# Performance work log

Measured on AMD Instinct MI355X. Metric: run time of the kernel, lower is better.

The kernel has to match this reference:

```python
import jax, jax.numpy as jnp
import numpy as np

N_TOKEN = 267735
D_EMBED = 1024
D_PROJ = 1024
CUTOFF_ENDS = [0, 20000, 40000, 200000, N_TOKEN]
DIV_VAL = 4
INIT_STD = 0.02


def setup_inputs() -> dict:
    key = jax.random.key(0)
    ks = jax.random.split(key, 9)
    inp = jax.random.randint(ks[0], (8, 4096), 0, N_TOKEN, dtype=jnp.int64)
    out = {"inp": inp}
    for i in range(4):
        l, r = CUTOFF_ENDS[i], CUTOFF_ENDS[i + 1]
        d_emb_i = D_EMBED // (DIV_VAL ** i)
        out[f"emb{i}"] = jax.random.normal(ks[1 + i], (r - l, d_emb_i), dtype=jnp.float32) * INIT_STD
        out[f"proj{i}"] = jax.random.normal(ks[5 + i], (d_emb_i, D_PROJ), dtype=jnp.float32) * INIT_STD
    return out


def reference(inp, emb0, emb1, emb2, emb3, proj0, proj1, proj2, proj3):
    embs = [emb0, emb1, emb2, emb3]
    projs = [proj0, proj1, proj2, proj3]
    flat = inp.reshape(-1)  # [N]
    out = jnp.zeros((flat.shape[0], D_PROJ), dtype=jnp.float32)
    for i in range(4):
        l, r = CUTOFF_ENDS[i], CUTOFF_ENDS[i + 1]
        mask = (flat >= l) & (flat < r)  # [N]
        idx = jnp.clip(flat - l, 0, r - l - 1)  # in-range even for out-of-bucket tokens
        e = embs[i][idx]                         # [N, d_emb_i] gather
        p = jnp.einsum('id,de->ie', e, projs[i])  # [N, D_PROJ]
        out = out + jnp.where(mask[:, None], p, 0.0)
    emb_scale = D_PROJ ** 0.5
    return (out * emb_scale).reshape(inp.shape + (D_PROJ,))
```

## Files before the change

kernel.cpp:

```cpp
#include <hip/hip_runtime.h>
#include <hip/hip_bf16.h>

#define N_TOK   32768
#define DPROJ   1024
#define SCALE   32.0f

typedef short bf16x8 __attribute__((ext_vector_type(8)));
typedef float f32x4  __attribute__((ext_vector_type(4)));

__device__ __forceinline__ short f2bf(float f) {
    unsigned u = __builtin_bit_cast(unsigned, f);
    unsigned r = (u + 0x7FFFu + ((u >> 16) & 1u)) >> 16;
    return (short)r;
}

__global__ void k_prep(const int* __restrict__ inp, int* __restrict__ cnt,
                       int* __restrict__ perm, int* __restrict__ rowidx,
                       const float* __restrict__ p0, const float* __restrict__ p1,
                       const float* __restrict__ p2, const float* __restrict__ p3,
                       short* __restrict__ t0, short* __restrict__ t1,
                       short* __restrict__ t2, short* __restrict__ t3)
{
    __shared__ float tile[128][17];

    if (blockIdx.x < 128) {
        int i = blockIdx.x * 256 + threadIdx.x;
        int t = inp[i];
        int b, l;
        if (t < 20000)       { b = 0; l = 0; }
        else if (t < 40000)  { b = 1; l = 20000; }
        else if (t < 200000) { b = 2; l = 40000; }
        else                 { b = 3; l = 200000; }

        unsigned long long m0 = __ballot(b == 0);
        unsigned long long m1 = __ballot(b == 1);
        unsigned long long m2 = __ballot(b == 2);
        unsigned long long m3 = __ballot(b == 3);

        int lane = threadIdx.x & 63;
        int mybase = 0;
        if (lane < 4) {
            unsigned long long mm = (lane == 0) ? m0 : (lane == 1) ? m1 : (lane == 2) ? m2 : m3;
            mybase = atomicAdd(&cnt[lane], __popcll(mm));
        }
        int base = __shfl(mybase, b);
        unsigned long long mine = (b == 0) ? m0 : (b == 1) ? m1 : (b == 2) ? m2 : m3;
        unsigned long long lt = (lane == 0) ? 0ull : (~0ull >> (64 - lane));
        int pos = base + __popcll(mine & lt);
        perm[b * N_TOK + pos]   = i;
        rowidx[b * N_TOK + pos] = t - l;
        return;
    }

    int bid = blockIdx.x - 128;
    const float* src; short* dst; int K; int rel;
    if (bid < 512)      { src = p0; dst = t0; K = 1024; rel = bid; }
    else if (bid < 640) { src = p1; dst = t1; K = 256;  rel = bid - 512; }
    else if (bid < 704) { src = p2; dst = t2; K = 64;   rel = bid - 640; }
    else                { src = p3; dst = t3; K = 16;   rel = bid - 704; }
    int ktiles = (K + 127) >> 7;
    int k0 = (rel % ktiles) * 128;
    int n0 = (rel / ktiles) * 16;
    int t = threadIdx.x;

    #pragma unroll
    for (int i = 0; i < 2; ++i) {
        int idx = t + i * 256;
        int k = idx >> 2;
        int nc = (idx & 3) * 4;
        if (k0 + k < K) {
            float4 v = *reinterpret_cast<const float4*>(src + (size_t)(k0 + k) * DPROJ + n0 + nc);
            tile[k][nc + 0] = v.x; tile[k][nc + 1] = v.y;
            tile[k][nc + 2] = v.z; tile[k][nc + 3] = v.w;
        }
    }
    __syncthreads();
    int n  = t >> 4;
    int kc = (t & 15) * 8;
    if (k0 + kc < K) {
        short s[8];
        #pragma unroll
        for (int j = 0; j < 8; ++j) s[j] = f2bf(tile[kc + j][n]);
        *reinterpret_cast<int4*>(dst + (size_t)(n0 + n) * K + k0 + kc) =
            *reinterpret_cast<const int4*>(s);
    }
}

__global__ __launch_bounds__(256, 2) void k_gemm(
    const float* __restrict__ e0, const float* __restrict__ e1,
    const float* __restrict__ e2, const float* __restrict__ e3,
    const short* __restrict__ t0, const short* __restrict__ t1,
    const short* __restrict__ t2, const short* __restrict__ t3,
    const int* __restrict__ cnt, const int* __restrict__ perm,
    const int* __restrict__ rowidx, float* __restrict__ out)
{
    __shared__ short As[64][40];
    __shared__ short Bs[256][40];

    const int hw     = blockIdx.y * 4 + blockIdx.x;
    const int ytile  = (hw >> 5) * 8 + (hw & 7);
    const int panel  = (hw >> 3) & 3;

    const int c0 = cnt[0], c1 = cnt[1], c2 = cnt[2], c3 = cnt[3];
    const int q0 = (c0 + 63) & ~63;
    const int q1 = q0 + ((c1 + 63) & ~63);
    const int q2 = q1 + ((c2 + 63) & ~63);
    const int q3 = q2 + ((c3 + 63) & ~63);
    const int p0 = ytile * 64;
    if (p0 >= q3) return;
    int b, M, m0, K; const float* emb; const short* bt;
    if (p0 < q0)      { b = 0; M = c0; m0 = p0;      K = 1024; emb = e0; bt = t0; }
    else if (p0 < q1) { b = 1; M = c1; m0 = p0 - q0; K = 256;  emb = e1; bt = t1; }
    else if (p0 < q2) { b = 2; M = c2; m0 = p0 - q1; K = 64;   emb = e2; bt = t2; }
    else              { b = 3; M = c3; m0 = p0 - q2; K = 16;   emb = e3; bt = t3; }
    if (m0 >= M) return;
    const int* pperm = perm   + b * N_TOK;
    const int* prow  = rowidx + b * N_TOK;

    const int tid  = threadIdx.x;
    const int lane = tid & 63;
    const int w    = tid >> 6;
    const int n0   = panel * 256;

    const int sr = tid >> 2;
    const int sc = (tid & 3) * 8;
    const bool avalid = (m0 + sr) < M;
    const int  arow   = avalid ? prow[m0 + sr] : 0;
    const float* aptr = emb + (size_t)arow * K;

    f32x4 acc[4][4];
    #pragma unroll
    for (int mi = 0; mi < 4; ++mi)
        #pragma unroll
        for (int ni = 0; ni < 4; ++ni) acc[mi][ni] = (f32x4)0.0f;

    const int koff = (lane >> 4) * 8;
    const int fr   = lane & 15;

    float av[8];
    int4  bv[4];
#define ISSUE_LOADS(K0)                                                        \
    {                                                                          \
        _Pragma("unroll")                                                      \
        for (int j = 0; j < 8; ++j) av[j] = 0.0f;                              \
        if (avalid && ((K0) + sc) < K) {                                       \
            float4 x = *reinterpret_cast<const float4*>(aptr + (K0) + sc);     \
            float4 y = *reinterpret_cast<const float4*>(aptr + (K0) + sc + 4); \
            av[0] = x.x; av[1] = x.y; av[2] = x.z; av[3] = x.w;                \
            av[4] = y.x; av[5] = y.y; av[6] = y.z; av[7] = y.w;                \
        }                                                                      \
        _Pragma("unroll")                                                      \
        for (int g = 0; g < 4; ++g) {                                          \
            if (((K0) + sc) < K)                                               \
                bv[g] = *reinterpret_cast<const int4*>(                        \
                    bt + (size_t)(n0 + g * 64 + sr) * K + (K0) + sc);          \
            else bv[g] = make_int4(0, 0, 0, 0);                                \
        }                                                                      \
    }

    ISSUE_LOADS(0);
    for (int k0 = 0; k0 < K; k0 += 32) {
        __syncthreads();
        {
            short asv[8];
            #pragma unroll
            for (int j = 0; j < 8; ++j) asv[j] = f2bf(av[j]);
            *reinterpret_cast<int4*>(&As[sr][sc]) = *reinterpret_cast<const int4*>(asv);
            #pragma unroll
            for (int g = 0; g < 4; ++g)
                *reinterpret_cast<int4*>(&Bs[g * 64 + sr][sc]) = bv[g];
        }
        if (k0 + 32 < K) ISSUE_LOADS(k0 + 32);
        __syncthreads();

        bf16x8 afr[4], bfr[4];
        #pragma unroll
        for (int mi = 0; mi < 4; ++mi)
            afr[mi] = *reinterpret_cast<const bf16x8*>(&As[mi * 16 + fr][koff]);
        #pragma unroll
        for (int ni = 0; ni < 4; ++ni)
            bfr[ni] = *reinterpret_cast<const bf16x8*>(&Bs[w * 64 + ni * 16 + fr][koff]);
        #pragma unroll
        for (int mi = 0; mi < 4; ++mi)
            #pragma unroll
            for (int ni = 0; ni < 4; ++ni)
                acc[mi][ni] = __builtin_amdgcn_mfma_f32_16x16x32_bf16(
                    afr[mi], bfr[ni], acc[mi][ni], 0, 0, 0);
    }
#undef ISSUE_LOADS

    const int colb = n0 + w * 64 + fr;
    const int rowg = (lane >> 4) * 4;
    #pragma unroll
    for (int mi = 0; mi < 4; ++mi) {
        #pragma unroll
        for (int j = 0; j < 4; ++j) {
            int m = m0 + mi * 16 + rowg + j;
            if (m < M) {
                size_t r = (size_t)pperm[m] * DPROJ + colb;
                out[r]      = acc[mi][0][j] * SCALE;
                out[r + 16] = acc[mi][1][j] * SCALE;
                out[r + 32] = acc[mi][2][j] * SCALE;
                out[r + 48] = acc[mi][3][j] * SCALE;
            }
        }
    }
}

__global__ void k_naive(const int* __restrict__ inp,
                        const float* __restrict__ emb0, const float* __restrict__ emb1,
                        const float* __restrict__ emb2, const float* __restrict__ emb3,
                        const float* __restrict__ proj0, const float* __restrict__ proj1,
                        const float* __restrict__ proj2, const float* __restrict__ proj3,
                        float* __restrict__ out)
{
    __shared__ float e[1024];
    int t = inp[blockIdx.x];
    const float* emb; const float* proj; int K, l;
    if (t < 20000)       { emb = emb0; proj = proj0; K = 1024; l = 0; }
    else if (t < 40000)  { emb = emb1; proj = proj1; K = 256;  l = 20000; }
    else if (t < 200000) { emb = emb2; proj = proj2; K = 64;   l = 40000; }
    else                 { emb = emb3; proj = proj3; K = 16;   l = 200000; }
    int tid = threadIdx.x;
    for (int k = tid; k < K; k += 256) e[k] = emb[(size_t)(t - l) * K + k];
    __syncthreads();
    float acc[4] = {0.f, 0.f, 0.f, 0.f};
    for (int k = 0; k < K; ++k) {
        float ek = e[k];
        #pragma unroll
        for (int c = 0; c < 4; ++c)
            acc[c] = fmaf(ek, proj[(size_t)k * DPROJ + tid + 256 * c], acc[c]);
    }
    #pragma unroll
    for (int c = 0; c < 4; ++c)
        out[(size_t)blockIdx.x * DPROJ + tid + 256 * c] = acc[c] * SCALE;
}

extern "C" void kernel_launch(void* const* d_in, const int* in_sizes, int n_in,
                              void* d_out, int out_size, void* d_ws, size_t ws_size,
                              hipStream_t stream) {
    const int*   inp   = (const int*)d_in[0];
    const float* emb0  = (const float*)d_in[1];
    const float* proj0 = (const float*)d_in[2];
    const float* emb1  = (const float*)d_in[3];
    const float* proj1 = (const float*)d_in[4];
    const float* emb2  = (const float*)d_in[5];
    const float* proj2 = (const float*)d_in[6];
    const float* emb3  = (const float*)d_in[7];
    const float* proj3 = (const float*)d_in[8];
    float* out = (float*)d_out;

    const size_t off_cnt  = 0;
    const size_t off_perm = 256;
    const size_t off_row  = off_perm + 4ull * N_TOK * 4;
    const size_t off_t0   = off_row  + 4ull * N_TOK * 4;
    const size_t off_t1   = off_t0 + 1024ull * 1024 * 2;
    const size_t off_t2   = off_t1 + 1024ull * 256 * 2;
    const size_t off_t3   = off_t2 + 1024ull * 64 * 2;
    const size_t needed   = off_t3 + 1024ull * 16 * 2;

    if (d_ws == nullptr || ws_size < needed) {
        k_naive<<<N_TOK, 256, 0, stream>>>(inp, emb0, emb1, emb2, emb3,
                                           proj0, proj1, proj2, proj3, out);
        return;
    }

    char* ws = (char*)d_ws;
    int*   cnt    = (int*)(ws + off_cnt);
    int*   perm   = (int*)(ws + off_perm);
    int*   rowidx = (int*)(ws + off_row);
    short* t0     = (short*)(ws + off_t0);
    short* t1     = (short*)(ws + off_t1);
    short* t2     = (short*)(ws + off_t2);
    short* t3     = (short*)(ws + off_t3);

    hipMemsetAsync(cnt, 0, 16, stream);
    k_prep<<<896, 256, 0, stream>>>(inp, cnt, perm, rowidx,
                                    proj0, proj1, proj2, proj3, t0, t1, t2, t3);

    dim3 grid(4, 520);
    k_gemm<<<grid, 256, 0, stream>>>(emb0, emb1, emb2, emb3,
                                     t0, t1, t2, t3,
                                     cnt, perm, rowidx, out);
}
```

Measured before the change: 55.82 us.

## Load B fragments directly from global and double-buffer A in LDS

The B-operand staging through shared memory is removed. Each wave now loads its bf16 B fragments straight from global memory into registers, and only the A tile (gathered embeddings converted to bf16) goes through LDS, now double-buffered so each k-step needs one barrier instead of two. The smaller LDS footprint lets occupancy rise to 3 blocks per SM via launch bounds. The trade is that B fragment loads are strided per lane (16-byte rows across K) and no longer reused through LDS, so there is more global and L2 traffic and B load latency sits directly ahead of the MFMAs.

```diff
diff --git a/kernel.cpp b/kernel.cpp
--- a/kernel.cpp
+++ b/kernel.cpp
@@ -86,7 +86,7 @@
     }
 }
 
-__global__ __launch_bounds__(256, 2) void k_gemm(
+__global__ __launch_bounds__(256, 3) void k_gemm(
     const float* __restrict__ e0, const float* __restrict__ e1,
     const float* __restrict__ e2, const float* __restrict__ e3,
     const short* __restrict__ t0, const short* __restrict__ t1,
@@ -94,8 +94,7 @@
     const int* __restrict__ cnt, const int* __restrict__ perm,
     const int* __restrict__ rowidx, float* __restrict__ out)
 {
-    __shared__ short As[64][40];
-    __shared__ short Bs[256][40];
+    __shared__ short As[2][64][40];
 
     const int hw     = blockIdx.y * 4 + blockIdx.x;
     const int ytile  = (hw >> 5) * 8 + (hw & 7);
@@ -136,10 +135,10 @@
 
     const int koff = (lane >> 4) * 8;
     const int fr   = lane & 15;
+    const short* btw = bt + (size_t)(n0 + w * 64 + fr) * K;
 
     float av[8];
-    int4  bv[4];
-#define ISSUE_LOADS(K0)                                                        \
+#define ISSUE_A(K0)                                                            \
     {                                                                          \
         _Pragma("unroll")                                                      \
         for (int j = 0; j < 8; ++j) av[j] = 0.0f;                              \
@@ -149,45 +148,51 @@
             av[0] = x.x; av[1] = x.y; av[2] = x.z; av[3] = x.w;                \
             av[4] = y.x; av[5] = y.y; av[6] = y.z; av[7] = y.w;                \
         }                                                                      \
+    }
+#define WRITE_A(BUF)                                                           \
+    {                                                                          \
+        short asv[8];                                                          \
         _Pragma("unroll")                                                      \
-        for (int g = 0; g < 4; ++g) {                                          \
-            if (((K0) + sc) < K)                                               \
-                bv[g] = *reinterpret_cast<const int4*>(                        \
-                    bt + (size_t)(n0 + g * 64 + sr) * K + (K0) + sc);          \
-            else bv[g] = make_int4(0, 0, 0, 0);                                \
-        }                                                                      \
-    }
-
-    ISSUE_LOADS(0);
-    for (int k0 = 0; k0 < K; k0 += 32) {
-        __syncthreads();
-        {
-            short asv[8];
-            #pragma unroll
-            for (int j = 0; j < 8; ++j) asv[j] = f2bf(av[j]);
-            *reinterpret_cast<int4*>(&As[sr][sc]) = *reinterpret_cast<const int4*>(asv);
-            #pragma unroll
-            for (int g = 0; g < 4; ++g)
-                *reinterpret_cast<int4*>(&Bs[g * 64 + sr][sc]) = bv[g];
-        }
-        if (k0 + 32 < K) ISSUE_LOADS(k0 + 32);
-        __syncthreads();
-
-        bf16x8 afr[4], bfr[4];
+        for (int j = 0; j < 8; ++j) asv[j] = f2bf(av[j]);                      \
+        *reinterpret_cast<int4*>(&As[BUF][sr][sc]) =                           \
+            *reinterpret_cast<const int4*>(asv);                               \
+    }
+
+    ISSUE_A(0);
+    WRITE_A(0);
+    __syncthreads();
+
+    int cur = 0;
+    for (int k0 = 0; k0 < K; k0 += 32, cur ^= 1) {
+        const bool more = (k0 + 32) < K;
+        if (more) ISSUE_A(k0 + 32);
+
+        bf16x8 bfr[4];
+        #pragma unroll
+        for (int ni = 0; ni < 4; ++ni) {
+            if ((k0 + koff) < K)
+                bfr[ni] = *reinterpret_cast<const bf16x8*>(
+                    btw + (size_t)ni * 16 * K + k0 + koff);
+            else
+                bfr[ni] = (bf16x8)0;
+        }
+        bf16x8 afr[4];
         #pragma unroll
         for (int mi = 0; mi < 4; ++mi)
-            afr[mi] = *reinterpret_cast<const bf16x8*>(&As[mi * 16 + fr][koff]);
-        #pragma unroll
-        for (int ni = 0; ni < 4; ++ni)
-            bfr[ni] = *reinterpret_cast<const bf16x8*>(&Bs[w * 64 + ni * 16 + fr][koff]);
+            afr[mi] = *reinterpret_cast<const bf16x8*>(&As[cur][mi * 16 + fr][koff]);
+
         #pragma unroll
         for (int mi = 0; mi < 4; ++mi)
             #pragma unroll
             for (int ni = 0; ni < 4; ++ni)
                 acc[mi][ni] = __builtin_amdgcn_mfma_f32_16x16x32_bf16(
                     afr[mi], bfr[ni], acc[mi][ni], 0, 0, 0);
-    }
-#undef ISSUE_LOADS
+
+        if (more) WRITE_A(cur ^ 1);
+        __syncthreads();
+    }
+#undef ISSUE_A
+#undef WRITE_A
 
     const int colb = n0 + w * 64 + fr;
     const int rowg = (lane >> 4) * 4;
```

Measured after the change: 65.19 us. +16.8%, slower.

## Specialize GEMM per bucket K and batch small-K buckets over four M-tiles

Applied to the files above, without the earlier changes.

Splits the gather-GEMM into templated bodies per bucket: deep buckets (K=1024, 256) keep the pipelined K loop without bounds checks, and shallow buckets (K=64, 16) load the projection panel into LDS once and loop over up to four 64-row M tiles with double-buffered A prefetch. The output scale of 32 is folded into the transposed bf16 projection during prep, and output row indices are preloaded. Launch bounds go to 3 blocks per CU. This aims to cut redundant B-panel loads and per-block overhead for the many small-K tiles, at the cost of idle blocks that return early and more register and LDS pressure.

```diff
diff --git a/kernel.cpp b/kernel.cpp
--- a/kernel.cpp
+++ b/kernel.cpp
@@ -13,6 +13,8 @@
     unsigned r = (u + 0x7FFFu + ((u >> 16) & 1u)) >> 16;
     return (short)r;
 }
+
+__device__ __forceinline__ int imin(int a, int b) { return a < b ? a : b; }
 
 __global__ void k_prep(const int* __restrict__ inp, int* __restrict__ cnt,
                        int* __restrict__ perm, int* __restrict__ rowidx,
@@ -80,13 +82,276 @@
     if (k0 + kc < K) {
         short s[8];
         #pragma unroll
-        for (int j = 0; j < 8; ++j) s[j] = f2bf(tile[kc + j][n]);
+        for (int j = 0; j < 8; ++j) s[j] = f2bf(tile[kc + j][n] * 32.0f);
         *reinterpret_cast<int4*>(dst + (size_t)(n0 + n) * K + k0 + kc) =
             *reinterpret_cast<const int4*>(s);
     }
 }
 
-__global__ __launch_bounds__(256, 2) void k_gemm(
+template<int K>
+__device__ __forceinline__ void body_deep(
+    const float* __restrict__ emb, const short* __restrict__ bt,
+    int M, int m0, const int* __restrict__ pperm, const int* __restrict__ prow,
+    int n0, float* __restrict__ out,
+    short (*As)[40], short (*Bs)[40])
+{
+    const int tid  = threadIdx.x;
+    const int lane = tid & 63;
+    const int w    = tid >> 6;
+    const int sr   = tid >> 2;
+    const int sc   = (tid & 3) * 8;
+    const bool avalid = (m0 + sr) < M;
+    const int  arow   = avalid ? prow[m0 + sr] : 0;
+    const float* aptr = emb + (size_t)arow * K;
+
+    const int koff = (lane >> 4) * 8;
+    const int fr   = lane & 15;
+    const int rowg = (lane >> 4) * 4;
+
+    int pr[4][4];
+    #pragma unroll
+    for (int mi = 0; mi < 4; ++mi)
+        #pragma unroll
+        for (int j = 0; j < 4; ++j) {
+            int m = m0 + mi * 16 + rowg + j;
+            pr[mi][j] = (m < M) ? pperm[m] : 0;
+        }
+
+    f32x4 acc[4][4];
+    #pragma unroll
+    for (int mi = 0; mi < 4; ++mi)
+        #pragma unroll
+        for (int ni = 0; ni < 4; ++ni) acc[mi][ni] = (f32x4)0.0f;
+
+    float av[8];
+    int4  bv[4];
+#define ISSUE_LOADS(K0)                                                        \
+    {                                                                          \
+        if (avalid) {                                                          \
+            float4 x = *reinterpret_cast<const float4*>(aptr + (K0) + sc);     \
+            float4 y = *reinterpret_cast<const float4*>(aptr + (K0) + sc + 4); \
+            av[0] = x.x; av[1] = x.y; av[2] = x.z; av[3] = x.w;                \
+            av[4] = y.x; av[5] = y.y; av[6] = y.z; av[7] = y.w;                \
+        } else {                                                               \
+            _Pragma("unroll")                                                  \
+            for (int j = 0; j < 8; ++j) av[j] = 0.0f;                          \
+        }                                                                      \
+        _Pragma("unroll")                                                      \
+        for (int g = 0; g < 4; ++g)                                            \
+            bv[g] = *reinterpret_cast<const int4*>(                            \
+                bt + (size_t)(n0 + g * 64 + sr) * K + (K0) + sc);              \
+    }
+
+    ISSUE_LOADS(0);
+    for (int k0 = 0; k0 < K; k0 += 32) {
+        __syncthreads();
+        {
+            short asv[8];
+            #pragma unroll
+            for (int j = 0; j < 8; ++j) asv[j] = f2bf(av[j]);
+            *reinterpret_cast<int4*>(&As[sr][sc]) = *reinterpret_cast<const int4*>(asv);
+            #pragma unroll
+            for (int g = 0; g < 4; ++g)
+                *reinterpret_cast<int4*>(&Bs[g * 64 + sr][sc]) = bv[g];
+        }
+        if (k0 + 32 < K) ISSUE_LOADS(k0 + 32);
+        __syncthreads();
+
+        bf16x8 afr[4], bfr[4];
+        #pragma unroll
+        for (int mi = 0; mi < 4; ++mi)
+            afr[mi] = *reinterpret_cast<const bf16x8*>(&As[mi * 16 + fr][koff]);
+        #pragma unroll
+        for (int ni = 0; ni < 4; ++ni)
+            bfr[ni] = *reinterpret_cast<const bf16x8*>(&Bs[w * 64 + ni * 16 + fr][koff]);
+        #pragma unroll
+        for (int mi = 0; mi < 4; ++mi)
+            #pragma unroll
+            for (int ni = 0; ni < 4; ++ni)
+                acc[mi][ni] = __builtin_amdgcn_mfma_f32_16x16x32_bf16(
+                    afr[mi], bfr[ni], acc[mi][ni], 0, 0, 0);
+    }
+#undef ISSUE_LOADS
+
+    const int colb = n0 + w * 64 + fr;
+    #pragma unroll
+    for (int mi = 0; mi < 4; ++mi) {
+        #pragma unroll
+        for (int j = 0; j < 4; ++j) {
+            int m = m0 + mi * 16 + rowg + j;
+            if (m < M) {
+                size_t r = (size_t)pr[mi][j] * DPROJ + colb;
+                out[r]      = acc[mi][0][j];
+                out[r + 16] = acc[mi][1][j];
+                out[r + 32] = acc[mi][2][j];
+                out[r + 48] = acc[mi][3][j];
+            }
+        }
+    }
+}
+
+template<int K>
+__device__ __forceinline__ void body_short4(
+    const float* __restrict__ emb, const short* __restrict__ bt,
+    int M, int m0base, int nt,
+    const int* __restrict__ pperm, const int* __restrict__ prow,
+    int n0, float* __restrict__ out, short* __restrict__ lds)
+{
+    short (*Bres)[68] = reinterpret_cast<short(*)[68]>(lds);
+    short (*As0)[68]  = reinterpret_cast<short(*)[68]>(lds + 17408);
+    short (*As1)[68]  = reinterpret_cast<short(*)[68]>(lds + 21760);
+
+    const int tid  = threadIdx.x;
+    const int lane = tid & 63;
+    const int w    = tid >> 6;
+    const int koff = (lane >> 4) * 8;
+    const int fr   = lane & 15;
+    const int rowg = (lane >> 4) * 4;
+
+    const int arow = tid >> 2;
+    const int ac   = (tid & 3) * ((K == 64) ? 16 : 4);
+
+    int rid[4];
+    #pragma unroll
+    for (int t = 0; t < 4; ++t) {
+        int m = m0base + t * 64 + arow;
+        rid[t] = (t < nt && m < M) ? prow[m] : 0;
+    }
+
+    #pragma unroll
+    for (int g = 0; g < 4; ++g) {
+        int row = g * 64 + (tid >> 2);
+        if constexpr (K == 64) {
+            const short* bp = bt + (size_t)(n0 + row) * 64 + (tid & 3) * 16;
+            *reinterpret_cast<int4*>(&Bres[row][(tid & 3) * 16])     =
+                *reinterpret_cast<const int4*>(bp);
+            *reinterpret_cast<int4*>(&Bres[row][(tid & 3) * 16 + 8]) =
+                *reinterpret_cast<const int4*>(bp + 8);
+        } else {
+            *reinterpret_cast<int2*>(&Bres[row][(tid & 3) * 4]) =
+                *reinterpret_cast<const int2*>(bt + (size_t)(n0 + row) * 16 + (tid & 3) * 4);
+        }
+    }
+
+    float4 aS0[4], aS1[4];
+    {
+        const float* ap = emb + (size_t)rid[0] * K + ac;
+        if constexpr (K == 64) {
+            #pragma unroll
+            for (int q = 0; q < 4; ++q)
+                aS0[q] = *reinterpret_cast<const float4*>(ap + q * 4);
+        } else {
+            aS0[0] = *reinterpret_cast<const float4*>(ap);
+        }
+    }
+
+    #pragma unroll
+    for (int t = 0; t < 4; ++t) {
+        if (t >= nt) break;
+        const int m0t = m0base + t * 64;
+        short (*AsP)[68] = ((t & 1) == 0) ? As0 : As1;
+
+        if constexpr (K == 64) {
+            const float4* src = ((t & 1) == 0) ? aS0 : aS1;
+            short s[16];
+            #pragma unroll
+            for (int q = 0; q < 4; ++q) {
+                s[q*4+0] = f2bf(src[q].x); s[q*4+1] = f2bf(src[q].y);
+                s[q*4+2] = f2bf(src[q].z); s[q*4+3] = f2bf(src[q].w);
+            }
+            *reinterpret_cast<int4*>(&AsP[arow][ac])     = *reinterpret_cast<const int4*>(s);
+            *reinterpret_cast<int4*>(&AsP[arow][ac + 8]) = *reinterpret_cast<const int4*>(s + 8);
+        } else {
+            const float4 v = ((t & 1) == 0) ? aS0[0] : aS1[0];
+            short s[4];
+            s[0] = f2bf(v.x); s[1] = f2bf(v.y); s[2] = f2bf(v.z); s[3] = f2bf(v.w);
+            *reinterpret_cast<int2*>(&AsP[arow][ac]) = *reinterpret_cast<const int2*>(s);
+            int z[2] = {0, 0};
+            *reinterpret_cast<int2*>(&AsP[arow][16 + ac]) = *reinterpret_cast<const int2*>(z);
+        }
+
+        if (t + 1 < nt) {
+            const float* ap = emb + (size_t)rid[t + 1] * K + ac;
+            if constexpr (K == 64) {
+                if ((t & 1) == 0) {
+                    #pragma unroll
+                    for (int q = 0; q < 4; ++q)
+                        aS1[q] = *reinterpret_cast<const float4*>(ap + q * 4);
+                } else {
+                    #pragma unroll
+                    for (int q = 0; q < 4; ++q)
+                        aS0[q] = *reinterpret_cast<const float4*>(ap + q * 4);
+                }
+            } else {
+                if ((t & 1) == 0) aS1[0] = *reinterpret_cast<const float4*>(ap);
+                else              aS0[0] = *reinterpret_cast<const float4*>(ap);
+            }
+        }
+
+        int pr[4][4];
+        #pragma unroll
+        for (int mi = 0; mi < 4; ++mi)
+            #pragma unroll
+            for (int j = 0; j < 4; ++j) {
+                int m = m0t + mi * 16 + rowg + j;
+                pr[mi][j] = (m < M) ? pperm[m] : 0;
+            }
+
+        __syncthreads();
+
+        bf16x8 b0[4], b1[4];
+        #pragma unroll
+        for (int ni = 0; ni < 4; ++ni) {
+            if (K == 16 && koff >= 16) {
+                b0[ni] = (bf16x8)0;
+            } else {
+                b0[ni] = *reinterpret_cast<const bf16x8*>(&Bres[w * 64 + ni * 16 + fr][koff]);
+            }
+            if constexpr (K == 64)
+                b1[ni] = *reinterpret_cast<const bf16x8*>(&Bres[w * 64 + ni * 16 + fr][32 + koff]);
+        }
+
+        f32x4 acc[4][4];
+        #pragma unroll
+        for (int mi = 0; mi < 4; ++mi)
+            #pragma unroll
+            for (int ni = 0; ni < 4; ++ni) acc[mi][ni] = (f32x4)0.0f;
+
+        #pragma unroll
+        for (int mi = 0; mi < 4; ++mi) {
+            bf16x8 a0 = *reinterpret_cast<const bf16x8*>(&AsP[mi * 16 + fr][koff]);
+            #pragma unroll
+            for (int ni = 0; ni < 4; ++ni)
+                acc[mi][ni] = __builtin_amdgcn_mfma_f32_16x16x32_bf16(
+                    a0, b0[ni], acc[mi][ni], 0, 0, 0);
+            if constexpr (K == 64) {
+                bf16x8 a1 = *reinterpret_cast<const bf16x8*>(&AsP[mi * 16 + fr][32 + koff]);
+                #pragma unroll
+                for (int ni = 0; ni < 4; ++ni)
+                    acc[mi][ni] = __builtin_amdgcn_mfma_f32_16x16x32_bf16(
+                        a1, b1[ni], acc[mi][ni], 0, 0, 0);
+            }
+        }
+
+        const int colb = n0 + w * 64 + fr;
+        #pragma unroll
+        for (int mi = 0; mi < 4; ++mi) {
+            #pragma unroll
+            for (int j = 0; j < 4; ++j) {
+                int m = m0t + mi * 16 + rowg + j;
+                if (m < M) {
+                    size_t r = (size_t)pr[mi][j] * DPROJ + colb;
+                    out[r]      = acc[mi][0][j];
+                    out[r + 16] = acc[mi][1][j];
+                    out[r + 32] = acc[mi][2][j];
+                    out[r + 48] = acc[mi][3][j];
+                }
+            }
+        }
+    }
+}
+
+__global__ __launch_bounds__(256, 3) void k_gemm(
     const float* __restrict__ e0, const float* __restrict__ e1,
     const float* __restrict__ e2, const float* __restrict__ e3,
     const short* __restrict__ t0, const short* __restrict__ t1,
@@ -94,12 +359,11 @@
     const int* __restrict__ cnt, const int* __restrict__ perm,
     const int* __restrict__ rowidx, float* __restrict__ out)
 {
-    __shared__ short As[64][40];
-    __shared__ short Bs[256][40];
-
-    const int hw     = blockIdx.y * 4 + blockIdx.x;
-    const int ytile  = (hw >> 5) * 8 + (hw & 7);
-    const int panel  = (hw >> 3) & 3;
+    __shared__ short lds[26112];
+
+    const int hw    = blockIdx.y * 4 + blockIdx.x;
+    const int ytile = (hw >> 5) * 8 + (hw & 7);
+    const int panel = (hw >> 3) & 3;
 
     const int c0 = cnt[0], c1 = cnt[1], c2 = cnt[2], c3 = cnt[3];
     const int q0 = (c0 + 63) & ~63;
@@ -108,102 +372,30 @@
     const int q3 = q2 + ((c3 + 63) & ~63);
     const int p0 = ytile * 64;
     if (p0 >= q3) return;
-    int b, M, m0, K; const float* emb; const short* bt;
-    if (p0 < q0)      { b = 0; M = c0; m0 = p0;      K = 1024; emb = e0; bt = t0; }
-    else if (p0 < q1) { b = 1; M = c1; m0 = p0 - q0; K = 256;  emb = e1; bt = t1; }
-    else if (p0 < q2) { b = 2; M = c2; m0 = p0 - q1; K = 64;   emb = e2; bt = t2; }
-    else              { b = 3; M = c3; m0 = p0 - q2; K = 16;   emb = e3; bt = t3; }
-    if (m0 >= M) return;
-    const int* pperm = perm   + b * N_TOK;
-    const int* prow  = rowidx + b * N_TOK;
-
-    const int tid  = threadIdx.x;
-    const int lane = tid & 63;
-    const int w    = tid >> 6;
-    const int n0   = panel * 256;
-
-    const int sr = tid >> 2;
-    const int sc = (tid & 3) * 8;
-    const bool avalid = (m0 + sr) < M;
-    const int  arow   = avalid ? prow[m0 + sr] : 0;
-    const float* aptr = emb + (size_t)arow * K;
-
-    f32x4 acc[4][4];
-    #pragma unroll
-    for (int mi = 0; mi < 4; ++mi)
-        #pragma unroll
-        for (int ni = 0; ni < 4; ++ni) acc[mi][ni] = (f32x4)0.0f;
-
-    const int koff = (lane >> 4) * 8;
-    const int fr   = lane & 15;
-
-    float av[8];
-    int4  bv[4];
-#define ISSUE_LOADS(K0)                                                        \
-    {                                                                          \
-        _Pragma("unroll")                                                      \
-        for (int j = 0; j < 8; ++j) av[j] = 0.0f;                              \
-        if (avalid && ((K0) + sc) < K) {                                       \
-            float4 x = *reinterpret_cast<const float4*>(aptr + (K0) + sc);     \
-            float4 y = *reinterpret_cast<const float4*>(aptr + (K0) + sc + 4); \
-            av[0] = x.x; av[1] = x.y; av[2] = x.z; av[3] = x.w;                \
-            av[4] = y.x; av[5] = y.y; av[6] = y.z; av[7] = y.w;                \
-        }                                                                      \
-        _Pragma("unroll")                                                      \
-        for (int g = 0; g < 4; ++g) {                                          \
-            if (((K0) + sc) < K)                                               \
-                bv[g] = *reinterpret_cast<const int4*>(                        \
-                    bt + (size_t)(n0 + g * 64 + sr) * K + (K0) + sc);          \
-            else bv[g] = make_int4(0, 0, 0, 0);                                \
-        }                                                                      \
-    }
-
-    ISSUE_LOADS(0);
-    for (int k0 = 0; k0 < K; k0 += 32) {
-        __syncthreads();
-        {
-            short asv[8];
-            #pragma unroll
-            for (int j = 0; j < 8; ++j) asv[j] = f2bf(av[j]);
-            *reinterpret_cast<int4*>(&As[sr][sc]) = *reinterpret_cast<const int4*>(asv);
-            #pragma unroll
-            for (int g = 0; g < 4; ++g)
-                *reinterpret_cast<int4*>(&Bs[g * 64 + sr][sc]) = bv[g];
-        }
-        if (k0 + 32 < K) ISSUE_LOADS(k0 + 32);
-        __syncthreads();
-
-        bf16x8 afr[4], bfr[4];
-        #pragma unroll
-        for (int mi = 0; mi < 4; ++mi)
-            afr[mi] = *reinterpret_cast<const bf16x8*>(&As[mi * 16 + fr][koff]);
-        #pragma unroll
-        for (int ni = 0; ni < 4; ++ni)
-            bfr[ni] = *reinterpret_cast<const bf16x8*>(&Bs[w * 64 + ni * 16 + fr][koff]);
-        #pragma unroll
-        for (int mi = 0; mi < 4; ++mi)
-            #pragma unroll
-            for (int ni = 0; ni < 4; ++ni)
-                acc[mi][ni] = __builtin_amdgcn_mfma_f32_16x16x32_bf16(
-                    afr[mi], bfr[ni], acc[mi][ni], 0, 0, 0);
-    }
-#undef ISSUE_LOADS
-
-    const int colb = n0 + w * 64 + fr;
-    const int rowg = (lane >> 4) * 4;
-    #pragma unroll
-    for (int mi = 0; mi < 4; ++mi) {
-        #pragma unroll
-        for (int j = 0; j < 4; ++j) {
-            int m = m0 + mi * 16 + rowg + j;
-            if (m < M) {
-                size_t r = (size_t)pperm[m] * DPROJ + colb;
-                out[r]      = acc[mi][0][j] * SCALE;
-                out[r + 16] = acc[mi][1][j] * SCALE;
-                out[r + 32] = acc[mi][2][j] * SCALE;
-                out[r + 48] = acc[mi][3][j] * SCALE;
-            }
-        }
+    const int n0 = panel * 256;
+
+    if (p0 < q0) {
+        body_deep<1024>(e0, t0, c0, p0, perm, rowidx, n0, out,
+                        reinterpret_cast<short(*)[40]>(lds),
+                        reinterpret_cast<short(*)[40]>(lds + 2560));
+    } else if (p0 < q1) {
+        body_deep<256>(e1, t1, c1, p0 - q0, perm + N_TOK, rowidx + N_TOK, n0, out,
+                       reinterpret_cast<short(*)[40]>(lds),
+                       reinterpret_cast<short(*)[40]>(lds + 2560));
+    } else if (p0 < q2) {
+        const int s = q1 >> 6;
+        if ((ytile - s) & 3) return;
+        const int e = q2 >> 6;
+        const int nt = imin(4, e - ytile);
+        body_short4<64>(e2, t2, c2, p0 - q1, nt,
+                        perm + 2 * N_TOK, rowidx + 2 * N_TOK, n0, out, lds);
+    } else {
+        const int s = q2 >> 6;
+        if ((ytile - s) & 3) return;
+        const int e = q3 >> 6;
+        const int nt = imin(4, e - ytile);
+        body_short4<16>(e3, t3, c3, p0 - q2, nt,
+                        perm + 3 * N_TOK, rowidx + 3 * N_TOK, n0, out, lds);
     }
 }
 
```

Result: slower. 115.0 us (+105.9%).
